# Optimization experiments

Measured on AMD Instinct MI355X. Metric: run time of the kernel, lower is better.

Reference implementation:

```python
import jax, jax.numpy as jnp
import numpy as np

B, N, H, W = 4, 256, 256, 256  # N == H required by the original code's view()

def setup_inputs() -> dict:
    key = jax.random.key(0)
    k1, k2, k3, k4, k5 = jax.random.split(key, 5)
    predictions = jax.random.normal(k1, (B, H, W), dtype=jnp.float32)
    # exactly one center per (b, n) channel
    cr = jax.random.randint(k2, (B, N), 0, H)
    cc = jax.random.randint(k3, (B, N), 0, W)
    bi = jnp.arange(B)[:, None] * jnp.ones((1, N), jnp.int32)
    ni = jnp.arange(N)[None, :] * jnp.ones((B, 1), jnp.int32)
    target_centers = jnp.zeros((B, N, H, W), jnp.int32).at[bi, ni, cr, cc].set(1)
    targets = jax.random.randint(k4, (B, N, H, W), 0, 2).astype(jnp.int32)
    pad_mask = jax.random.randint(k5, (B, N), 0, 2).astype(jnp.bool_)
    return {"predictions": predictions, "target_centers": target_centers,
            "targets": targets, "pad_mask": pad_mask}

def reference(predictions, target_centers, targets, pad_mask):
    b, n, h, w = targets.shape
    # extract the (unique) center coordinate of each channel (replaces torch.where)
    flat_idx = jnp.argmax(target_centers.reshape(b, n, h * w), axis=-1)  # [B,N]
    center_rows = flat_idx // w
    center_cols = flat_idx % w
    rows = jnp.arange(h, dtype=jnp.int32)[:, None]   # [H,1]
    cols = jnp.arange(w, dtype=jnp.int32)[None, :]   # [1,W]
    # broadcast per-pixel squared distance to each channel's center: [B,N,H,W]
    squared_dist = ((rows[None, None] - center_rows[:, :, None, None]) ** 2
                    + (cols[None, None] - center_cols[:, :, None, None]) ** 2)
    pixel_importance = targets.astype(jnp.float32) / (squared_dist.astype(jnp.float32) + 1e-6)
    pixel_importance = jnp.where(pad_mask[:, :, None, None], 0.0, pixel_importance)
    pixel_importance = pixel_importance.sum(axis=1)  # [B,H,W]
    tsum = targets.sum(axis=1)                        # int, [B,H,W]
    importance_coeff = jnp.invert(tsum).astype(jnp.float32) * 0.5  # torch ~int semantics
    pixel_importance = pixel_importance + importance_coeff
    z = tsum.astype(jnp.float32)
    x = predictions
    # BCE with logits, stable form (matches F.binary_cross_entropy_with_logits)
    bce = jnp.maximum(x, 0.0) - x * z + jnp.log1p(jnp.exp(-jnp.abs(x)))
    return jnp.mean(bce * pixel_importance)
```

## Files before the change

### kernel.cpp

```cpp
#include <hip/hip_runtime.h>
#include <stdint.h>

#define BATCH 4
#define NCH   256
#define HH    256
#define WW    256
#define HWSZ  (HH * WW)
#define NPIX  (BATCH * HWSZ)

__global__ __launch_bounds__(256) void find_centers(
    const int* __restrict__ tc, int* __restrict__ centers)
{
    const int bn  = blockIdx.x;
    const int tid = threadIdx.x;
    const int4* p = (const int4*)(tc + (size_t)bn * HWSZ);

    int found = -1;
    #pragma unroll 4
    for (int i = 0; i < HWSZ / 4 / 256; ++i) {
        const int idx = i * 256 + tid;
        const int4 v = p[idx];
        if (v.x | v.y | v.z | v.w) {
            int off = v.x ? 0 : (v.y ? 1 : (v.z ? 2 : 3));
            found = idx * 4 + off;
        }
    }
    if (found >= 0) centers[bn] = found;
}

__global__ __launch_bounds__(256) void loss_kernel(
    const float* __restrict__ pred,
    const int*   __restrict__ targets,
    const unsigned char* __restrict__ padraw,
    const int*   __restrict__ centers,
    float*       __restrict__ out)
{
    __shared__ int   cpack[NCH];
    __shared__ int   modeflag;
    __shared__ float wsum[4];

    const int tid = threadIdx.x;
    if (tid == 0) modeflag = 0;
    __syncthreads();

    {
        const unsigned int wv = ((const unsigned int*)padraw)[tid];
        if (wv & 0xFFFFFF00u) modeflag = 1;
    }
    __syncthreads();

    const int b  = blockIdx.x >> 7;
    const int h0 = (blockIdx.x & 127) << 1;

    {
        const int n = tid;
        const int cidx = centers[b * NCH + n];
        int pad;
        if (modeflag) pad = (padraw[b * NCH + n] != 0);
        else          pad = (((const int*)padraw)[b * NCH + n] != 0);
        cpack[n] = (cidx & 0xFFFF) | (pad << 30);
    }
    __syncthreads();

    const int hrow = h0 + (tid >> 7);
    const int wcol = (tid & 127) << 1;

    const int* base = targets + (size_t)b * NCH * HWSZ + hrow * WW + wcol;

    int   tsum0 = 0, tsum1 = 0;
    float imp0 = 0.f, imp1 = 0.f;

    #pragma unroll 8
    for (int n = 0; n < NCH; ++n) {
        const int2 v = *(const int2*)(base + (size_t)n * HWSZ);
        const int c  = cpack[n];
        const int cr = (c >> 8) & 255;
        const int cc = c & 255;
        const int dh  = hrow - cr;
        const int dw0 = wcol - cc;
        const int dw1 = dw0 + 1;
        const int dh2 = dh * dh;
        const float f0 = (float)(dh2 + dw0 * dw0) + 1e-6f;
        const float f1 = (float)(dh2 + dw1 * dw1) + 1e-6f;
        tsum0 += v.x;
        tsum1 += v.y;
        const int valid = ((c & (1 << 30)) == 0);
        if (v.x & valid) imp0 += __builtin_amdgcn_rcpf(f0);
        if (v.y & valid) imp1 += __builtin_amdgcn_rcpf(f1);
    }

    const float it0 = imp0 + (float)(~tsum0) * 0.5f;
    const float it1 = imp1 + (float)(~tsum1) * 0.5f;

    const int pix = b * HWSZ + hrow * WW + wcol;
    const float x0 = pred[pix];
    const float x1 = pred[pix + 1];
    const float bce0 = fmaxf(x0, 0.f) - x0 * (float)tsum0 + log1pf(expf(-fabsf(x0)));
    const float bce1 = fmaxf(x1, 0.f) - x1 * (float)tsum1 + log1pf(expf(-fabsf(x1)));

    float contrib = bce0 * it0 + bce1 * it1;

    #pragma unroll
    for (int o = 32; o > 0; o >>= 1) contrib += __shfl_down(contrib, o, 64);
    const int wave = tid >> 6;
    if ((tid & 63) == 0) wsum[wave] = contrib;
    __syncthreads();
    if (tid == 0) {
        const float s = wsum[0] + wsum[1] + wsum[2] + wsum[3];
        atomicAdd(out, s * (1.0f / (float)NPIX));
    }
}

extern "C" void kernel_launch(void* const* d_in, const int* in_sizes, int n_in,
                              void* d_out, int out_size, void* d_ws, size_t ws_size,
                              hipStream_t stream)
{
    const float* pred = (const float*)d_in[0];
    const int*   tc   = (const int*)d_in[1];
    const int*   tg   = (const int*)d_in[2];
    const unsigned char* pm = (const unsigned char*)d_in[3];
    float* out   = (float*)d_out;
    int* centers = (int*)d_ws;

    hipMemsetAsync(d_out, 0, sizeof(float), stream);
    find_centers<<<BATCH * NCH, 256, 0, stream>>>(tc, centers);
    loss_kernel<<<BATCH * HH / 2, 256, 0, stream>>>(pred, tg, pm, centers, out);
}
```

Baseline: 592.1 us.

## Precompute per-row distance terms in LDS and process one pixel per thread

Each block now handles a single image row, one pixel per thread, and launches twice as many blocks. Per-channel shared data is reduced to a float pair holding the precomputed dh^2+eps (infinity for padded channels) and the center column. The inner loop then needs only an FMA, a reciprocal and an FMA with no branches, replacing the earlier integer unpacking and masking. This cuts ALU work per element but drops the int2 vector loads in favour of scalar 4-byte loads, and the find_centers unroll is raised.

```diff
diff --git a/kernel.cpp b/kernel.cpp
--- a/kernel.cpp
+++ b/kernel.cpp
@@ -16,7 +16,7 @@
     const int4* p = (const int4*)(tc + (size_t)bn * HWSZ);
 
     int found = -1;
-    #pragma unroll 4
+    #pragma unroll 8
     for (int i = 0; i < HWSZ / 4 / 256; ++i) {
         const int idx = i * 256 + tid;
         const int4 v = p[idx];
@@ -35,9 +35,9 @@
     const int*   __restrict__ centers,
     float*       __restrict__ out)
 {
-    __shared__ int   cpack[NCH];
-    __shared__ int   modeflag;
-    __shared__ float wsum[4];
+    __shared__ float2 cinfo[NCH];
+    __shared__ int    modeflag;
+    __shared__ float  wsum[4];
 
     const int tid = threadIdx.x;
     if (tid == 0) modeflag = 0;
@@ -49,56 +49,46 @@
     }
     __syncthreads();
 
-    const int b  = blockIdx.x >> 7;
-    const int h0 = (blockIdx.x & 127) << 1;
+    const int b    = blockIdx.x >> 8;
+    const int hrow = blockIdx.x & 255;
 
     {
-        const int n = tid;
+        const int n    = tid;
         const int cidx = centers[b * NCH + n];
+        const int cr   = cidx >> 8;
+        const int cc   = cidx & 255;
         int pad;
         if (modeflag) pad = (padraw[b * NCH + n] != 0);
         else          pad = (((const int*)padraw)[b * NCH + n] != 0);
-        cpack[n] = (cidx & 0xFFFF) | (pad << 30);
+        const int dh = hrow - cr;
+        float fdh2e = (float)(dh * dh) + 1e-6f;
+        if (pad) fdh2e = __builtin_inff();
+        cinfo[n] = make_float2(fdh2e, (float)cc);
     }
     __syncthreads();
 
-    const int hrow = h0 + (tid >> 7);
-    const int wcol = (tid & 127) << 1;
+    const float wcolf = (float)tid;
+    const int* base = targets + (size_t)b * NCH * HWSZ + hrow * WW + tid;
 
-    const int* base = targets + (size_t)b * NCH * HWSZ + hrow * WW + wcol;
+    int   tsum = 0;
+    float imp  = 0.f;
 
-    int   tsum0 = 0, tsum1 = 0;
-    float imp0 = 0.f, imp1 = 0.f;
-
-    #pragma unroll 8
+    #pragma unroll 16
     for (int n = 0; n < NCH; ++n) {
-        const int2 v = *(const int2*)(base + (size_t)n * HWSZ);
-        const int c  = cpack[n];
-        const int cr = (c >> 8) & 255;
-        const int cc = c & 255;
-        const int dh  = hrow - cr;
-        const int dw0 = wcol - cc;
-        const int dw1 = dw0 + 1;
-        const int dh2 = dh * dh;
-        const float f0 = (float)(dh2 + dw0 * dw0) + 1e-6f;
-        const float f1 = (float)(dh2 + dw1 * dw1) + 1e-6f;
-        tsum0 += v.x;
-        tsum1 += v.y;
-        const int valid = ((c & (1 << 30)) == 0);
-        if (v.x & valid) imp0 += __builtin_amdgcn_rcpf(f0);
-        if (v.y & valid) imp1 += __builtin_amdgcn_rcpf(f1);
+        const int    v = base[(size_t)n * HWSZ];
+        const float2 c = cinfo[n];
+        const float fdw = wcolf - c.y;
+        const float f   = __builtin_fmaf(fdw, fdw, c.x);
+        imp = __builtin_fmaf((float)v, __builtin_amdgcn_rcpf(f), imp);
+        tsum += v;
     }
 
-    const float it0 = imp0 + (float)(~tsum0) * 0.5f;
-    const float it1 = imp1 + (float)(~tsum1) * 0.5f;
+    const float it = __builtin_fmaf((float)(~tsum), 0.5f, imp);
 
-    const int pix = b * HWSZ + hrow * WW + wcol;
-    const float x0 = pred[pix];
-    const float x1 = pred[pix + 1];
-    const float bce0 = fmaxf(x0, 0.f) - x0 * (float)tsum0 + log1pf(expf(-fabsf(x0)));
-    const float bce1 = fmaxf(x1, 0.f) - x1 * (float)tsum1 + log1pf(expf(-fabsf(x1)));
+    const float x   = pred[b * HWSZ + hrow * WW + tid];
+    const float bce = fmaxf(x, 0.f) - x * (float)tsum + log1pf(expf(-fabsf(x)));
 
-    float contrib = bce0 * it0 + bce1 * it1;
+    float contrib = bce * it;
 
     #pragma unroll
     for (int o = 32; o > 0; o >>= 1) contrib += __shfl_down(contrib, o, 64);
@@ -124,5 +114,5 @@
 
     hipMemsetAsync(d_out, 0, sizeof(float), stream);
     find_centers<<<BATCH * NCH, 256, 0, stream>>>(tc, centers);
-    loss_kernel<<<BATCH * HH / 2, 256, 0, stream>>>(pred, tg, pm, centers, out);
+    loss_kernel<<<BATCH * HH, 256, 0, stream>>>(pred, tg, pm, centers, out);
 }
```

Measured after the change: 508.5 us. 1.16x faster.
